# Performance work log

Measured on AMD Instinct MI355X. Metric: run time of the kernel, lower is better.

The kernel has to match this reference:

```python
import jax, jax.numpy as jnp
import numpy as np

DIM, D_INNER, D_STATE, DT_RANK, D_CONV = 1024, 2048, 16, 64, 4
BATCH, SEQ = 2, 1024

def setup_inputs() -> dict:
    key = jax.random.key(0)
    ks = jax.random.split(key, 9)
    s = 0.02
    A = jnp.tile(jnp.arange(1, D_STATE + 1, dtype=jnp.float32), (D_INNER, 1))
    return {
        "x": jax.random.normal(ks[0], (BATCH, SEQ, DIM), jnp.float32),
        "in_proj_w": jax.random.normal(ks[1], (DIM, 2 * D_INNER), jnp.float32) * s,
        "conv_w": jax.random.normal(ks[2], (D_INNER, 1, D_CONV), jnp.float32) * 0.2,
        "conv_b": jax.random.normal(ks[3], (D_INNER,), jnp.float32) * 0.1,
        "x_proj_w": jax.random.normal(ks[4], (D_INNER, DT_RANK + 2 * D_STATE), jnp.float32) * s,
        "dt_proj_w": jax.random.normal(ks[5], (DT_RANK, D_INNER), jnp.float32) * s,
        "dt_proj_b": jax.random.normal(ks[6], (D_INNER,), jnp.float32) * 0.1,
        "A_log": jnp.log(A),
        "D_param": jnp.ones((D_INNER,), jnp.float32),
        "out_proj_w": jax.random.normal(ks[7], (D_INNER, DIM), jnp.float32) * s,
    }

def _silu(v):
    return v * jax.nn.sigmoid(v)

def _ssm_forward(x, in_proj_w, conv_w, conv_b, x_proj_w, dt_proj_w, dt_proj_b, A_log, D_param, out_proj_w):
    b, l, _ = x.shape
    d_inner, d_conv = conv_w.shape[0], conv_w.shape[2]
    dt_rank, n = dt_proj_w.shape[0], A_log.shape[1]
    # input projection and split into conv branch / gate branch
    x_and_res = x @ in_proj_w                      # (b, l, 2*d_inner)
    xp, res = x_and_res[..., :d_inner], x_and_res[..., d_inner:]
    # causal depthwise conv (torch pads d_conv-1 both sides then slices [:l])
    h = jax.lax.conv_general_dilated(
        xp.transpose(0, 2, 1), conv_w,
        window_strides=(1,), padding=[(d_conv - 1, 0)],
        dimension_numbers=("NCH", "OIH", "NCH"),
        feature_group_count=d_inner,
    ) + conv_b[None, :, None]                      # (b, d_inner, l)
    h = _silu(h.transpose(0, 2, 1))                # (b, l, d_inner)
    # input-dependent SSM parameters
    A = -jnp.exp(A_log)                            # (d_inner, n)
    x_dbl = h @ x_proj_w                           # (b, l, dt_rank + 2n)
    dlt, Bm, Cm = (x_dbl[..., :dt_rank],
                   x_dbl[..., dt_rank:dt_rank + n],
                   x_dbl[..., dt_rank + n:])
    delta = jax.nn.softplus(dlt @ dt_proj_w + dt_proj_b)   # (b, l, d_inner)
    # discretization
    deltaA = jnp.exp(jnp.einsum("bld,dn->bldn", delta, A))             # (b,l,d,n)
    deltaB_u = (delta * h)[..., None] * Bm[:, :, None, :]              # (b,l,d,n)
    # sequential selective scan over time via lax.scan
    def step(state, t):
        dA_t, dBu_t, c_t = t
        state = dA_t * state + dBu_t               # (b, d, n)
        y_t = jnp.einsum("bdn,bn->bd", state, c_t)
        return state, y_t
    init = jnp.zeros((b, d_inner, n), h.dtype)
    _, ys = jax.lax.scan(step, init,
                         (deltaA.transpose(1, 0, 2, 3),
                          deltaB_u.transpose(1, 0, 2, 3),
                          Cm.transpose(1, 0, 2)))
    y = ys.transpose(1, 0, 2) + h * D_param        # (b, l, d_inner)
    y = y * _silu(res)
    return y @ out_proj_w                          # (b, l, dim)

def reference(x, in_proj_w, conv_w, conv_b, x_proj_w, dt_proj_w, dt_proj_b, A_log, D_param, out_proj_w):
    return _ssm_forward(x, in_proj_w, conv_w, conv_b, x_proj_w, dt_proj_w, dt_proj_b, A_log, D_param, out_proj_w)
```

## Files before the change

kernel.cpp:

```cpp
#include <hip/hip_runtime.h>
#include <hip/hip_bf16.h>

#define DIM     1024
#define DINNER  2048
#define NSTATE  16
#define DTRANK  64
#define DCONV   4
#define BATCH   2
#define SEQ     1024
#define BL      (BATCH*SEQ)
#define XDBLW   96
#define NCHUNK  32
#define TCHUNK  32
#define KSLICE  16
#define G4SK    4
#define LOG2E   1.44269504088896f
#define LN2     0.69314718055995f

typedef __attribute__((ext_vector_type(4))) float  f32x4;
typedef __attribute__((ext_vector_type(8))) short  bf16x8;
typedef unsigned short ushort_t;

__device__ __forceinline__ ushort_t f2bf(float f) {
    union { float f; unsigned int u; } v; v.f = f;
    unsigned int lsb = (v.u >> 16) & 1u;
    v.u += 0x7fffu + lsb;
    return (ushort_t)(v.u >> 16);
}
__device__ __forceinline__ float bf2f(ushort_t h) {
    union { unsigned u; float f; } v; v.u = ((unsigned)h) << 16; return v.f;
}
__device__ __forceinline__ float hexp2(float x) { return __builtin_amdgcn_exp2f(x); }
__device__ __forceinline__ float hlog2(float x) { return __builtin_amdgcn_logf(x); }
__device__ __forceinline__ float hrcp(float x)  { return __builtin_amdgcn_rcpf(x); }
__device__ __forceinline__ float softplus_fast(float x) {
    float e = hexp2(-fabsf(x) * LOG2E);
    return fmaxf(x, 0.f) + LN2 * hlog2(1.f + e);
}
__device__ __forceinline__ float sigmoid_fast(float x) {
    return hrcp(1.f + hexp2(-x * LOG2E));
}

typedef __attribute__((address_space(1))) unsigned int gu32_t;
typedef __attribute__((address_space(3))) unsigned int lu32_t;
__device__ __forceinline__ void gload_lds16(const ushort_t* g, ushort_t* l) {
    __builtin_amdgcn_global_load_lds((const gu32_t*)(const void*)g,
                                     (lu32_t*)(void*)l, 16, 0, 0);
}

__global__ __launch_bounds__(256) void prep_fused(
    const float* __restrict__ Win,  ushort_t* __restrict__ WtIn,
    const float* __restrict__ Wout, ushort_t* __restrict__ WtOut,
    const float* __restrict__ Wxp,  ushort_t* __restrict__ WtXp,
    const float* __restrict__ x,    ushort_t* __restrict__ xb)
{
    __shared__ float tile[32][33];
    const int tid = threadIdx.x;
    const int tx = tid & 31, ty = tid >> 5;
    const int bid = blockIdx.x;

    const float* src; ushort_t* dst; int R, C, bx, by;
    if (bid < 4096)      { src = Win;  dst = WtIn;  R = 1024; C = 4096; int j = bid;        bx = j % 128; by = j / 128; }
    else if (bid < 6144) { src = Wout; dst = WtOut; R = 2048; C = 1024; int j = bid - 4096; bx = j % 32;  by = j / 32; }
    else if (bid < 6336) { src = Wxp;  dst = WtXp;  R = 2048; C = 96;   int j = bid - 6144; bx = j % 3;   by = j / 3; }
    else {
        int i = ((bid - 6336) * 256 + tid) * 4;
        f32x4 v = *(const f32x4*)(x + i);
        ushort_t r0 = f2bf(v[0]), r1 = f2bf(v[1]), r2 = f2bf(v[2]), r3 = f2bf(v[3]);
        *(uint2*)(xb + i) = make_uint2((unsigned)r0 | ((unsigned)r1 << 16),
                                       (unsigned)r2 | ((unsigned)r3 << 16));
        return;
    }

    const int r0 = by * 32, c0 = bx * 32;
    #pragma unroll
    for (int i = 0; i < 4; ++i)
        tile[ty + i * 8][tx] = src[(size_t)(r0 + ty + i * 8) * C + c0 + tx];
    __syncthreads();
    #pragma unroll
    for (int i = 0; i < 4; ++i)
        dst[(size_t)(c0 + ty + i * 8) * R + r0 + tx] = f2bf(tile[tx][ty + i * 8]);
}

__global__ __launch_bounds__(256) void gemm_lds(
    const ushort_t* __restrict__ A,  int lda,
    const ushort_t* __restrict__ Bt, int ldb,
    int K,
    float* __restrict__ Cf, ushort_t* __restrict__ Cb, int ldc)
{
    __shared__ ushort_t As[2][128 * 32];
    __shared__ ushort_t Bs[2][128 * 32];

    const int tid  = threadIdx.x;
    const int m0   = blockIdx.y * 128;
    const int n0   = blockIdx.x * 128;
    const int wid  = tid >> 6;
    const int lane = tid & 63;
    const int wm   = (wid >> 1) * 64;
    const int wn   = (wid & 1) * 64;
    const int lr   = lane & 15;
    const int lk   = (lane >> 4) * 8;

    const int c0 = wid * 64 + lane;
    const int c1 = 256 + c0;
    const int r0 = c0 >> 2, f0 = (c0 & 3) * 8;
    const int r1 = c1 >> 2, f1 = (c1 & 3) * 8;
    const int lo0 = (wid * 64) * 8;
    const int lo1 = (256 + wid * 64) * 8;

    f32x4 acc[4][4];
    #pragma unroll
    for (int m = 0; m < 4; ++m)
        #pragma unroll
        for (int n = 0; n < 4; ++n)
            acc[m][n] = (f32x4){0.f, 0.f, 0.f, 0.f};

    const int nk = K >> 5;

    gload_lds16(A  + (size_t)(m0 + r0) * lda + f0, &As[0][lo0]);
    gload_lds16(A  + (size_t)(m0 + r1) * lda + f1, &As[0][lo1]);
    gload_lds16(Bt + (size_t)(n0 + r0) * ldb + f0, &Bs[0][lo0]);
    gload_lds16(Bt + (size_t)(n0 + r1) * ldb + f1, &Bs[0][lo1]);

    for (int k = 0; k < nk; ++k) {
        const int cur = k & 1;
        if (k + 1 < nk) {
            const int k0 = (k + 1) << 5;
            gload_lds16(A  + (size_t)(m0 + r0) * lda + k0 + f0, &As[cur ^ 1][lo0]);
            gload_lds16(A  + (size_t)(m0 + r1) * lda + k0 + f1, &As[cur ^ 1][lo1]);
            gload_lds16(Bt + (size_t)(n0 + r0) * ldb + k0 + f0, &Bs[cur ^ 1][lo0]);
            gload_lds16(Bt + (size_t)(n0 + r1) * ldb + k0 + f1, &Bs[cur ^ 1][lo1]);
            asm volatile("s_waitcnt vmcnt(4)" ::: "memory");
        } else {
            asm volatile("s_waitcnt vmcnt(0)" ::: "memory");
        }
        __builtin_amdgcn_sched_barrier(0);
        __builtin_amdgcn_s_barrier();

        bf16x8 af[4], bfr[4];
        #pragma unroll
        for (int m = 0; m < 4; ++m)
            af[m] = *(const bf16x8*)(&As[cur][(wm + m * 16 + lr) * 32 + lk]);
        #pragma unroll
        for (int n = 0; n < 4; ++n)
            bfr[n] = *(const bf16x8*)(&Bs[cur][(wn + n * 16 + lr) * 32 + lk]);

        #pragma unroll
        for (int m = 0; m < 4; ++m)
            #pragma unroll
            for (int n = 0; n < 4; ++n)
                acc[m][n] = __builtin_amdgcn_mfma_f32_16x16x32_bf16(af[m], bfr[n], acc[m][n], 0, 0, 0);
        __builtin_amdgcn_s_barrier();
    }

    const int rbase = (lane >> 4) * 4;
    #pragma unroll
    for (int m = 0; m < 4; ++m) {
        #pragma unroll
        for (int n = 0; n < 4; ++n) {
            int col = n0 + wn + n * 16 + lr;
            #pragma unroll
            for (int r = 0; r < 4; ++r) {
                int row = m0 + wm + m * 16 + rbase + r;
                float v = acc[m][n][r];
                if (Cf) Cf[(size_t)row * ldc + col] = v;
                if (Cb) Cb[(size_t)row * ldc + col] = f2bf(v);
            }
        }
    }
}

__global__ __launch_bounds__(256) void gemm_lds_sk(
    const ushort_t* __restrict__ A,  int lda,
    const ushort_t* __restrict__ Bt, int ldb,
    int klen,
    float* __restrict__ Part, int ldc, int mn)
{
    __shared__ ushort_t As[2][128 * 32];
    __shared__ ushort_t Bs[2][128 * 32];

    const int tid  = threadIdx.x;
    const int m0   = blockIdx.y * 128;
    const int n0   = blockIdx.x * 128;
    const int kb   = blockIdx.z * klen;
    float* Cf = Part + (size_t)blockIdx.z * mn;

    const int wid  = tid >> 6;
    const int lane = tid & 63;
    const int wm   = (wid >> 1) * 64;
    const int wn   = (wid & 1) * 64;
    const int lr   = lane & 15;
    const int lk   = (lane >> 4) * 8;

    const int c0 = wid * 64 + lane;
    const int c1 = 256 + c0;
    const int r0 = c0 >> 2, f0 = (c0 & 3) * 8;
    const int r1 = c1 >> 2, f1 = (c1 & 3) * 8;
    const int lo0 = (wid * 64) * 8;
    const int lo1 = (256 + wid * 64) * 8;

    f32x4 acc[4][4];
    #pragma unroll
    for (int m = 0; m < 4; ++m)
        #pragma unroll
        for (int n = 0; n < 4; ++n)
            acc[m][n] = (f32x4){0.f, 0.f, 0.f, 0.f};

    const int nk = klen >> 5;

    gload_lds16(A  + (size_t)(m0 + r0) * lda + kb + f0, &As[0][lo0]);
    gload_lds16(A  + (size_t)(m0 + r1) * lda + kb + f1, &As[0][lo1]);
    gload_lds16(Bt + (size_t)(n0 + r0) * ldb + kb + f0, &Bs[0][lo0]);
    gload_lds16(Bt + (size_t)(n0 + r1) * ldb + kb + f1, &Bs[0][lo1]);

    for (int k = 0; k < nk; ++k) {
        const int cur = k & 1;
        if (k + 1 < nk) {
            const int k0 = kb + ((k + 1) << 5);
            gload_lds16(A  + (size_t)(m0 + r0) * lda + k0 + f0, &As[cur ^ 1][lo0]);
            gload_lds16(A  + (size_t)(m0 + r1) * lda + k0 + f1, &As[cur ^ 1][lo1]);
            gload_lds16(Bt + (size_t)(n0 + r0) * ldb + k0 + f0, &Bs[cur ^ 1][lo0]);
            gload_lds16(Bt + (size_t)(n0 + r1) * ldb + k0 + f1, &Bs[cur ^ 1][lo1]);
            asm volatile("s_waitcnt vmcnt(4)" ::: "memory");
        } else {
            asm volatile("s_waitcnt vmcnt(0)" ::: "memory");
        }
        __builtin_amdgcn_sched_barrier(0);
        __builtin_amdgcn_s_barrier();

        bf16x8 af[4], bfr[4];
        #pragma unroll
        for (int m = 0; m < 4; ++m)
            af[m] = *(const bf16x8*)(&As[cur][(wm + m * 16 + lr) * 32 + lk]);
        #pragma unroll
        for (int n = 0; n < 4; ++n)
            bfr[n] = *(const bf16x8*)(&Bs[cur][(wn + n * 16 + lr) * 32 + lk]);

        #pragma unroll
        for (int m = 0; m < 4; ++m)
            #pragma unroll
            for (int n = 0; n < 4; ++n)
                acc[m][n] = __builtin_amdgcn_mfma_f32_16x16x32_bf16(af[m], bfr[n], acc[m][n], 0, 0, 0);
        __builtin_amdgcn_s_barrier();
    }

    const int rbase = (lane >> 4) * 4;
    #pragma unroll
    for (int m = 0; m < 4; ++m) {
        #pragma unroll
        for (int n = 0; n < 4; ++n) {
            int col = n0 + wn + n * 16 + lr;
            #pragma unroll
            for (int r = 0; r < 4; ++r) {
                int row = m0 + wm + m * 16 + rbase + r;
                Cf[(size_t)row * ldc + col] = acc[m][n][r];
            }
        }
    }
}

__global__ __launch_bounds__(256) void g4_reduce(
    const float* __restrict__ Part, float* __restrict__ out)
{
    int i = (blockIdx.x * 256 + threadIdx.x) * 4;
    const size_t mn = (size_t)BL * DIM;
    f32x4 s = *(const f32x4*)(Part + i);
    #pragma unroll
    for (int z = 1; z < G4SK; ++z)
        s += *(const f32x4*)(Part + z * mn + i);
    *(f32x4*)(out + i) = s;
}

__global__ __launch_bounds__(256) void gemm_n96_splitk(
    const ushort_t* __restrict__ A,
    const ushort_t* __restrict__ Bt,
    float* __restrict__ Ppart)
{
    __shared__ ushort_t As[128 * 40];
    __shared__ ushort_t Bs[96 * 40];

    const int tid   = threadIdx.x;
    const int ks    = blockIdx.x;
    const int m0    = blockIdx.y * 128;
    const int kbase = ks * (DINNER / KSLICE);
    const int wid   = tid >> 6;
    const int lane  = tid & 63;
    const int wm    = wid * 32;
    const int lr    = lane & 15;
    const int lk    = (lane >> 4) * 8;

    f32x4 acc[2][6];
    #pragma unroll
    for (int m = 0; m < 2; ++m)
        #pragma unroll
        for (int n = 0; n < 6; ++n)
            acc[m][n] = (f32x4){0.f, 0.f, 0.f, 0.f};

    for (int k0 = kbase; k0 < kbase + DINNER / KSLICE; k0 += 32) {
        #pragma unroll
        for (int c = 0; c < 2; ++c) {
            int cid = tid + c * 256;
            int row = cid >> 2, ck = (cid & 3) * 8;
            *(uint4*)(&As[row * 40 + ck]) =
                *(const uint4*)(A + (size_t)(m0 + row) * DINNER + k0 + ck);
        }
        {
            int row = tid >> 2, ck = (tid & 3) * 8;
            *(uint4*)(&Bs[row * 40 + ck]) =
                *(const uint4*)(Bt + (size_t)row * DINNER + k0 + ck);
            if (tid < 128) {
                int cid = 256 + tid;
                int row2 = cid >> 2, ck2 = (cid & 3) * 8;
                *(uint4*)(&Bs[row2 * 40 + ck2]) =
                    *(const uint4*)(Bt + (size_t)row2 * DINNER + k0 + ck2);
            }
        }
        __syncthreads();

        bf16x8 af[2], bfr[6];
        #pragma unroll
        for (int m = 0; m < 2; ++m)
            af[m] = *(const bf16x8*)(&As[(wm + m * 16 + lr) * 40 + lk]);
        #pragma unroll
        for (int n = 0; n < 6; ++n)
            bfr[n] = *(const bf16x8*)(&Bs[(n * 16 + lr) * 40 + lk]);

        #pragma unroll
        for (int m = 0; m < 2; ++m)
            #pragma unroll
            for (int n = 0; n < 6; ++n)
                acc[m][n] = __builtin_amdgcn_mfma_f32_16x16x32_bf16(af[m], bfr[n], acc[m][n], 0, 0, 0);
        __syncthreads();
    }

    const int rbase = (lane >> 4) * 4;
    #pragma unroll
    for (int m = 0; m < 2; ++m) {
        #pragma unroll
        for (int n = 0; n < 6; ++n) {
            int col = n * 16 + lr;
            #pragma unroll
            for (int r = 0; r < 4; ++r) {
                int row = m0 + wm + m * 16 + rbase + r;
                Ppart[((size_t)ks * BL + row) * XDBLW + col] = acc[m][n][r];
            }
        }
    }
}

__global__ __launch_bounds__(256) void g2_reduce(
    const float* __restrict__ Ppart, float* __restrict__ xdbl)
{
    int idx = blockIdx.x * 256 + threadIdx.x;
    int row = idx / 24, cg = (idx % 24) * 4;
    f32x4 s = (f32x4){0.f, 0.f, 0.f, 0.f};
    #pragma unroll
    for (int ks = 0; ks < KSLICE; ++ks)
        s += *(const f32x4*)(Ppart + ((size_t)ks * BL + row) * XDBLW + cg);
    *(f32x4*)(xdbl + (size_t)row * XDBLW + cg) = s;
}

__global__ __launch_bounds__(256, 4) void delta_v6(
    const float* __restrict__ xdbl,
    const float* __restrict__ Wdt,
    const float* __restrict__ dtb,
    ushort_t* __restrict__ delta_bf)
{
    __shared__ float WS[64][256];
    __shared__ float dS[32][64];
    const int tid  = threadIdx.x;
    const int d0   = (blockIdx.x & 7) * 256;
    const int row0 = (blockIdx.x >> 3) * 32;

    #pragma unroll
    for (int i = 0; i < 16; ++i) {
        int c = i * 256 + tid;
        int k = c >> 6, co = (c & 63) * 4;
        *(f32x4*)&WS[k][co] = *(const f32x4*)(Wdt + (size_t)k * DINNER + d0 + co);
    }
    #pragma unroll
    for (int i = 0; i < 2; ++i) {
        int c = i * 256 + tid;
        int r = c >> 4, co = (c & 15) * 4;
        *(f32x4*)&dS[r][co] = *(const f32x4*)(xdbl + (size_t)(row0 + r) * XDBLW + co);
    }
    __syncthreads();

    const int w    = tid >> 6;
    const int lane = tid & 63;
    const int dd   = lane * 4;

    f32x4 acc[8];
    {
        f32x4 bb = *(const f32x4*)(dtb + d0 + dd);
        #pragma unroll
        for (int r = 0; r < 8; ++r) acc[r] = bb;
    }

    for (int kq = 0; kq < 16; ++kq) {
        f32x4 dv[8];
        #pragma unroll
        for (int r = 0; r < 8; ++r)
            dv[r] = *(const f32x4*)&dS[w * 8 + r][kq * 4];
        #pragma unroll
        for (int kk = 0; kk < 4; ++kk) {
            f32x4 wv = *(const f32x4*)&WS[kq * 4 + kk][dd];
            #pragma unroll
            for (int r = 0; r < 8; ++r) {
                float dk = dv[r][kk];
                acc[r][0] = fmaf(dk, wv[0], acc[r][0]);
                acc[r][1] = fmaf(dk, wv[1], acc[r][1]);
                acc[r][2] = fmaf(dk, wv[2], acc[r][2]);
                acc[r][3] = fmaf(dk, wv[3], acc[r][3]);
            }
        }
    }

    #pragma unroll
    for (int r = 0; r < 8; ++r) {
        const size_t rowb = (size_t)(row0 + w * 8 + r) * DINNER + d0;
        f32x4 v = acc[r];
        ushort_t o[4];
        #pragma unroll
        for (int j = 0; j < 4; ++j)
            o[j] = f2bf(softplus_fast(v[j]));
        *(uint2*)(delta_bf + rowb + dd) = make_uint2(
            (unsigned)o[0] | ((unsigned)o[1] << 16), (unsigned)o[2] | ((unsigned)o[3] << 16));
    }
}

__global__ __launch_bounds__(256) void conv_silu(
    const ushort_t* __restrict__ xrb,
    const float* __restrict__ convw,
    const float* __restrict__ convb,
    ushort_t* __restrict__ hb)
{
    const int d  = blockIdx.x * 256 + threadIdx.x;
    const int bt = blockIdx.y;
    const int t  = bt & (SEQ - 1);

    float acc = convb[d];
    #pragma unroll
    for (int j = 0; j < DCONV; ++j) {
        int tt = t + j - (DCONV - 1);
        if (tt >= 0)
            acc += convw[d * DCONV + j] * bf2f(xrb[(size_t)(bt + j - (DCONV - 1)) * 4096 + d]);
    }
    float h = acc * sigmoid_fast(acc);
    hb[(size_t)bt * DINNER + d] = f2bf(h);
}

__global__ __launch_bounds__(256) void scan_p1(
    const ushort_t* __restrict__ delta_bf,
    const ushort_t* __restrict__ hb,
    const float* __restrict__ xdbl,
    const float* __restrict__ Alog,
    float* __restrict__ Pbuf,
    float* __restrict__ Sbuf)
{
    const int d  = (blockIdx.x & 7) * 256 + threadIdx.x;
    const int bc = blockIdx.x >> 3;
    const int b  = bc >> 5;
    const int c  = bc & (NCHUNK - 1);
    const int t0 = c * TCHUNK;

    float A[NSTATE];
    #pragma unroll
    for (int q = 0; q < 4; ++q) {
        f32x4 al = *(const f32x4*)(Alog + (size_t)d * NSTATE + q * 4);
        #pragma unroll
        for (int j = 0; j < 4; ++j)
            A[q * 4 + j] = -hexp2(al[j] * LOG2E) * LOG2E;
    }

    float s[NSTATE], pp[NSTATE];
    #pragma unroll
    for (int n = 0; n < NSTATE; ++n) { s[n] = 0.f; pp[n] = 1.f; }

    for (int tt = 0; tt < TCHUNK; ++tt) {
        const size_t row = (size_t)(b * SEQ + t0 + tt);
        float dl = bf2f(delta_bf[row * DINNER + d]);
        float hv = bf2f(hb[row * DINNER + d]);
        float dlh = dl * hv;
        float Bv[NSTATE];
        #pragma unroll
        for (int q = 0; q < 4; ++q) {
            f32x4 bv = *(const f32x4*)(xdbl + row * XDBLW + DTRANK + q * 4);
            #pragma unroll
            for (int j = 0; j < 4; ++j) Bv[q * 4 + j] = bv[j];
        }
        #pragma unroll
        for (int n = 0; n < NSTATE; ++n) {
            float a = hexp2(dl * A[n]);
            s[n]  = fmaf(a, s[n], dlh * Bv[n]);
            pp[n] *= a;
        }
    }

    const size_t o = (((size_t)b * NCHUNK + c) * DINNER + d) * NSTATE;
    #pragma unroll
    for (int q = 0; q < 4; ++q) {
        *(f32x4*)(Sbuf + o + q * 4) = (f32x4){s[q*4+0], s[q*4+1], s[q*4+2], s[q*4+3]};
        *(f32x4*)(Pbuf + o + q * 4) = (f32x4){pp[q*4+0], pp[q*4+1], pp[q*4+2], pp[q*4+3]};
    }
}

__global__ __launch_bounds__(256) void scan_p2(
    const float* __restrict__ Pbuf, float* __restrict__ Sbuf)
{
    const int tid = blockIdx.x * 256 + threadIdx.x;
    const int n = tid & 15;
    const int d = (tid >> 4) & (DINNER - 1);
    const int b = tid >> 15;
    const size_t stride = (size_t)DINNER * NSTATE;
    size_t idx = ((size_t)b * NCHUNK * DINNER + d) * NSTATE + n;
    float cin = 0.f;
    for (int c = 0; c < NCHUNK; ++c, idx += stride) {
        float S = Sbuf[idx];
        float P = Pbuf[idx];
        Sbuf[idx] = cin;
        cin = fmaf(P, cin, S);
    }
}

__global__ __launch_bounds__(256) void scan_p3(
    const ushort_t* __restrict__ delta_bf,
    const ushort_t* __restrict__ hb,
    const float* __restrict__ xdbl,
    const ushort_t* __restrict__ xrb,
    const float* __restrict__ Alog,
    const float* __restrict__ Dp,
    const float* __restrict__ Sbuf,
    ushort_t* __restrict__ yb)
{
    const int d  = (blockIdx.x & 7) * 256 + threadIdx.x;
    const int bc = blockIdx.x >> 3;
    const int b  = bc >> 5;
    const int c  = bc & (NCHUNK - 1);
    const int t0 = c * TCHUNK;

    float A[NSTATE];
    #pragma unroll
    for (int q = 0; q < 4; ++q) {
        f32x4 al = *(const f32x4*)(Alog + (size_t)d * NSTATE + q * 4);
        #pragma unroll
        for (int j = 0; j < 4; ++j)
            A[q * 4 + j] = -hexp2(al[j] * LOG2E) * LOG2E;
    }
    const float Dd = Dp[d];

    float s[NSTATE];
    const size_t o = (((size_t)b * NCHUNK + c) * DINNER + d) * NSTATE;
    #pragma unroll
    for (int q = 0; q < 4; ++q) {
        f32x4 sv = *(const f32x4*)(Sbuf + o + q * 4);
        #pragma unroll
        for (int j = 0; j < 4; ++j) s[q * 4 + j] = sv[j];
    }

    for (int tt = 0; tt < TCHUNK; ++tt) {
        const size_t row = (size_t)(b * SEQ + t0 + tt);
        float dl = bf2f(delta_bf[row * DINNER + d]);
        float hv = bf2f(hb[row * DINNER + d]);
        float rv = bf2f(xrb[row * 4096 + DINNER + d]);
        float dlh = dl * hv;
        float Bv[NSTATE], Cv[NSTATE];
        #pragma unroll
        for (int q = 0; q < 4; ++q) {
            f32x4 bv = *(const f32x4*)(xdbl + row * XDBLW + DTRANK + q * 4);
            f32x4 cv = *(const f32x4*)(xdbl + row * XDBLW + DTRANK + NSTATE + q * 4);
            #pragma unroll
            for (int j = 0; j < 4; ++j) { Bv[q*4+j] = bv[j]; Cv[q*4+j] = cv[j]; }
        }
        float y = 0.f;
        #pragma unroll
        for (int n = 0; n < NSTATE; ++n) {
            float a = hexp2(dl * A[n]);
            s[n] = fmaf(a, s[n], dlh * Bv[n]);
            y = fmaf(s[n], Cv[n], y);
        }
        y = fmaf(hv, Dd, y);
        y = y * rv * sigmoid_fast(rv);
        yb[row * DINNER + d] = f2bf(y);
    }
}

extern "C" void kernel_launch(void* const* d_in, const int* in_sizes, int n_in,
                              void* d_out, int out_size, void* d_ws, size_t ws_size,
                              hipStream_t stream)
{
    const float* x     = (const float*)d_in[0];
    const float* Win   = (const float*)d_in[1];
    const float* convw = (const float*)d_in[2];
    const float* convb = (const float*)d_in[3];
    const float* Wxp   = (const float*)d_in[4];
    const float* Wdt   = (const float*)d_in[5];
    const float* dtb   = (const float*)d_in[6];
    const float* Alog  = (const float*)d_in[7];
    const float* Dp    = (const float*)d_in[8];
    const float* Wout  = (const float*)d_in[9];
    float* out = (float*)d_out;

    char* base = (char*)d_ws; size_t off = 0;
    auto alloc = [&](size_t bytes) -> char* {
        char* q = base + off;
        off = (off + bytes + 255) & ~(size_t)255;
        return q;
    };
    ushort_t* WtIn   = (ushort_t*)alloc((size_t)4096 * 1024 * 2);
    ushort_t* WtOut  = (ushort_t*)alloc((size_t)1024 * 2048 * 2);
    ushort_t* WtXp   = (ushort_t*)alloc((size_t)96   * 2048 * 2);
    ushort_t* xb     = (ushort_t*)alloc((size_t)BL * DIM * 2);
    ushort_t* xrb    = (ushort_t*)alloc((size_t)BL * 4096 * 2);
    ushort_t* hb     = (ushort_t*)alloc((size_t)BL * DINNER * 2);
    float*    xdbl   = (float*)   alloc((size_t)BL * XDBLW * 4);
    ushort_t* dltbf  = (ushort_t*)alloc((size_t)BL * DINNER * 2);
    ushort_t* yb     = (ushort_t*)alloc((size_t)BL * DINNER * 2);
    float*    Pbuf   = (float*)   alloc((size_t)BATCH * NCHUNK * DINNER * NSTATE * 4);
    float*    Sbuf   = (float*)   alloc((size_t)BATCH * NCHUNK * DINNER * NSTATE * 4);
    float*    Ppart  = (float*)   alloc((size_t)KSLICE * BL * XDBLW * 4);
    float*    G4part = (float*)   alloc((size_t)G4SK * BL * DIM * 4);
    (void)ws_size;

    prep_fused<<<dim3(8384), 256, 0, stream>>>(Win, WtIn, Wout, WtOut, Wxp, WtXp, x, xb);

    gemm_lds<<<dim3(4096/128, BL/128), 256, 0, stream>>>(
        xb, DIM, WtIn, DIM, DIM, nullptr, xrb, 2*DINNER);

    conv_silu<<<dim3(DINNER/256, BL), 256, 0, stream>>>(xrb, convw, convb, hb);

    gemm_n96_splitk<<<dim3(KSLICE, BL/128), 256, 0, stream>>>(hb, WtXp, Ppart);
    g2_reduce<<<dim3(BL * 24 / 256), 256, 0, stream>>>(Ppart, xdbl);

    delta_v6<<<dim3(8 * (BL / 32)), 256, 0, stream>>>(xdbl, Wdt, dtb, dltbf);

    scan_p1<<<dim3(8 * BATCH * NCHUNK), 256, 0, stream>>>(dltbf, hb, xdbl, Alog, Pbuf, Sbuf);
    scan_p2<<<dim3(BATCH * DINNER * NSTATE / 256), 256, 0, stream>>>(Pbuf, Sbuf);
    scan_p3<<<dim3(8 * BATCH * NCHUNK), 256, 0, stream>>>(dltbf, hb, xdbl, xrb, Alog, Dp, Sbuf, yb);

    gemm_lds_sk<<<dim3(DIM/128, BL/128, G4SK), 256, 0, stream>>>(
        yb, DINNER, WtOut, DINNER, DINNER/G4SK, G4part, DIM, BL*DIM);
    g4_reduce<<<dim3(BL*DIM/4/256), 256, 0, stream>>>(G4part, out);
}
```

Before: 154.5 us.

## Double GEMM K-tile to 64 with XOR-swizzled LDS layout

Both bf16 MFMA GEMM kernels now stage 64-wide K slices per iteration instead of 32, halving the number of barrier/wait rounds per K sweep. The global-to-LDS copies use an XOR swizzle of the 16-byte column group by row, and fragment reads apply the matching swizzle to avoid LDS bank conflicts with the wider 128-byte rows. LDS use doubles to 64 KB per block, which may reduce occupancy. K lengths must now be multiples of 64, including split-K slice lengths.

```diff
diff --git a/kernel.cpp b/kernel.cpp
--- a/kernel.cpp
+++ b/kernel.cpp
@@ -88,8 +88,8 @@
     int K,
     float* __restrict__ Cf, ushort_t* __restrict__ Cb, int ldc)
 {
-    __shared__ ushort_t As[2][128 * 32];
-    __shared__ ushort_t Bs[2][128 * 32];
+    __shared__ ushort_t As[2][128 * 64];
+    __shared__ ushort_t Bs[2][128 * 64];
 
     const int tid  = threadIdx.x;
     const int m0   = blockIdx.y * 128;
@@ -99,14 +99,15 @@
     const int wm   = (wid >> 1) * 64;
     const int wn   = (wid & 1) * 64;
     const int lr   = lane & 15;
-    const int lk   = (lane >> 4) * 8;
-
-    const int c0 = wid * 64 + lane;
-    const int c1 = 256 + c0;
-    const int r0 = c0 >> 2, f0 = (c0 & 3) * 8;
-    const int r1 = c1 >> 2, f1 = (c1 & 3) * 8;
-    const int lo0 = (wid * 64) * 8;
-    const int lo1 = (256 + wid * 64) * 8;
+
+    int rq[4], gq[4], lo[4];
+    #pragma unroll
+    for (int q = 0; q < 4; ++q) {
+        int c = q * 256 + tid;
+        rq[q] = c >> 3;
+        gq[q] = ((c & 7) ^ (rq[q] & 7)) * 8;
+        lo[q] = (q * 256 + wid * 64) * 8;
+    }
 
     f32x4 acc[4][4];
     #pragma unroll
@@ -115,41 +116,47 @@
         for (int n = 0; n < 4; ++n)
             acc[m][n] = (f32x4){0.f, 0.f, 0.f, 0.f};
 
-    const int nk = K >> 5;
-
-    gload_lds16(A  + (size_t)(m0 + r0) * lda + f0, &As[0][lo0]);
-    gload_lds16(A  + (size_t)(m0 + r1) * lda + f1, &As[0][lo1]);
-    gload_lds16(Bt + (size_t)(n0 + r0) * ldb + f0, &Bs[0][lo0]);
-    gload_lds16(Bt + (size_t)(n0 + r1) * ldb + f1, &Bs[0][lo1]);
+    const int nk = K >> 6;
+
+    #pragma unroll
+    for (int q = 0; q < 4; ++q) {
+        gload_lds16(A  + (size_t)(m0 + rq[q]) * lda + gq[q], &As[0][lo[q]]);
+        gload_lds16(Bt + (size_t)(n0 + rq[q]) * ldb + gq[q], &Bs[0][lo[q]]);
+    }
 
     for (int k = 0; k < nk; ++k) {
         const int cur = k & 1;
         if (k + 1 < nk) {
-            const int k0 = (k + 1) << 5;
-            gload_lds16(A  + (size_t)(m0 + r0) * lda + k0 + f0, &As[cur ^ 1][lo0]);
-            gload_lds16(A  + (size_t)(m0 + r1) * lda + k0 + f1, &As[cur ^ 1][lo1]);
-            gload_lds16(Bt + (size_t)(n0 + r0) * ldb + k0 + f0, &Bs[cur ^ 1][lo0]);
-            gload_lds16(Bt + (size_t)(n0 + r1) * ldb + k0 + f1, &Bs[cur ^ 1][lo1]);
-            asm volatile("s_waitcnt vmcnt(4)" ::: "memory");
+            const int k0 = (k + 1) << 6;
+            #pragma unroll
+            for (int q = 0; q < 4; ++q) {
+                gload_lds16(A  + (size_t)(m0 + rq[q]) * lda + k0 + gq[q], &As[cur ^ 1][lo[q]]);
+                gload_lds16(Bt + (size_t)(n0 + rq[q]) * ldb + k0 + gq[q], &Bs[cur ^ 1][lo[q]]);
+            }
+            asm volatile("s_waitcnt vmcnt(8)" ::: "memory");
         } else {
             asm volatile("s_waitcnt vmcnt(0)" ::: "memory");
         }
         __builtin_amdgcn_sched_barrier(0);
         __builtin_amdgcn_s_barrier();
 
-        bf16x8 af[4], bfr[4];
-        #pragma unroll
-        for (int m = 0; m < 4; ++m)
-            af[m] = *(const bf16x8*)(&As[cur][(wm + m * 16 + lr) * 32 + lk]);
-        #pragma unroll
-        for (int n = 0; n < 4; ++n)
-            bfr[n] = *(const bf16x8*)(&Bs[cur][(wn + n * 16 + lr) * 32 + lk]);
-
-        #pragma unroll
-        for (int m = 0; m < 4; ++m)
+        #pragma unroll
+        for (int kk = 0; kk < 2; ++kk) {
+            const int lg = (lane >> 4) + kk * 4;
+            const int pc = (lg ^ (lr & 7)) * 8;
+            bf16x8 af[4], bfr[4];
+            #pragma unroll
+            for (int m = 0; m < 4; ++m)
+                af[m] = *(const bf16x8*)(&As[cur][(wm + m * 16 + lr) * 64 + pc]);
             #pragma unroll
             for (int n = 0; n < 4; ++n)
-                acc[m][n] = __builtin_amdgcn_mfma_f32_16x16x32_bf16(af[m], bfr[n], acc[m][n], 0, 0, 0);
+                bfr[n] = *(const bf16x8*)(&Bs[cur][(wn + n * 16 + lr) * 64 + pc]);
+            #pragma unroll
+            for (int m = 0; m < 4; ++m)
+                #pragma unroll
+                for (int n = 0; n < 4; ++n)
+                    acc[m][n] = __builtin_amdgcn_mfma_f32_16x16x32_bf16(af[m], bfr[n], acc[m][n], 0, 0, 0);
+        }
         __builtin_amdgcn_s_barrier();
     }
 
@@ -176,8 +183,8 @@
     int klen,
     float* __restrict__ Part, int ldc, int mn)
 {
-    __shared__ ushort_t As[2][128 * 32];
-    __shared__ ushort_t Bs[2][128 * 32];
+    __shared__ ushort_t As[2][128 * 64];
+    __shared__ ushort_t Bs[2][128 * 64];
 
     const int tid  = threadIdx.x;
     const int m0   = blockIdx.y * 128;
@@ -190,14 +197,15 @@
     const int wm   = (wid >> 1) * 64;
     const int wn   = (wid & 1) * 64;
     const int lr   = lane & 15;
-    const int lk   = (lane >> 4) * 8;
-
-    const int c0 = wid * 64 + lane;
-    const int c1 = 256 + c0;
-    const int r0 = c0 >> 2, f0 = (c0 & 3) * 8;
-    const int r1 = c1 >> 2, f1 = (c1 & 3) * 8;
-    const int lo0 = (wid * 64) * 8;
-    const int lo1 = (256 + wid * 64) * 8;
+
+    int rq[4], gq[4], lo[4];
+    #pragma unroll
+    for (int q = 0; q < 4; ++q) {
+        int c = q * 256 + tid;
+        rq[q] = c >> 3;
+        gq[q] = ((c & 7) ^ (rq[q] & 7)) * 8;
+        lo[q] = (q * 256 + wid * 64) * 8;
+    }
 
     f32x4 acc[4][4];
     #pragma unroll
@@ -206,41 +214,47 @@
         for (int n = 0; n < 4; ++n)
             acc[m][n] = (f32x4){0.f, 0.f, 0.f, 0.f};
 
-    const int nk = klen >> 5;
-
-    gload_lds16(A  + (size_t)(m0 + r0) * lda + kb + f0, &As[0][lo0]);
-    gload_lds16(A  + (size_t)(m0 + r1) * lda + kb + f1, &As[0][lo1]);
-    gload_lds16(Bt + (size_t)(n0 + r0) * ldb + kb + f0, &Bs[0][lo0]);
-    gload_lds16(Bt + (size_t)(n0 + r1) * ldb + kb + f1, &Bs[0][lo1]);
+    const int nk = klen >> 6;
+
+    #pragma unroll
+    for (int q = 0; q < 4; ++q) {
+        gload_lds16(A  + (size_t)(m0 + rq[q]) * lda + kb + gq[q], &As[0][lo[q]]);
+        gload_lds16(Bt + (size_t)(n0 + rq[q]) * ldb + kb + gq[q], &Bs[0][lo[q]]);
+    }
 
     for (int k = 0; k < nk; ++k) {
         const int cur = k & 1;
         if (k + 1 < nk) {
-            const int k0 = kb + ((k + 1) << 5);
-            gload_lds16(A  + (size_t)(m0 + r0) * lda + k0 + f0, &As[cur ^ 1][lo0]);
-            gload_lds16(A  + (size_t)(m0 + r1) * lda + k0 + f1, &As[cur ^ 1][lo1]);
-            gload_lds16(Bt + (size_t)(n0 + r0) * ldb + k0 + f0, &Bs[cur ^ 1][lo0]);
-            gload_lds16(Bt + (size_t)(n0 + r1) * ldb + k0 + f1, &Bs[cur ^ 1][lo1]);
-            asm volatile("s_waitcnt vmcnt(4)" ::: "memory");
+            const int k0 = kb + ((k + 1) << 6);
+            #pragma unroll
+            for (int q = 0; q < 4; ++q) {
+                gload_lds16(A  + (size_t)(m0 + rq[q]) * lda + k0 + gq[q], &As[cur ^ 1][lo[q]]);
+                gload_lds16(Bt + (size_t)(n0 + rq[q]) * ldb + k0 + gq[q], &Bs[cur ^ 1][lo[q]]);
+            }
+            asm volatile("s_waitcnt vmcnt(8)" ::: "memory");
         } else {
             asm volatile("s_waitcnt vmcnt(0)" ::: "memory");
         }
         __builtin_amdgcn_sched_barrier(0);
         __builtin_amdgcn_s_barrier();
 
-        bf16x8 af[4], bfr[4];
-        #pragma unroll
-        for (int m = 0; m < 4; ++m)
-            af[m] = *(const bf16x8*)(&As[cur][(wm + m * 16 + lr) * 32 + lk]);
-        #pragma unroll
-        for (int n = 0; n < 4; ++n)
-            bfr[n] = *(const bf16x8*)(&Bs[cur][(wn + n * 16 + lr) * 32 + lk]);
-
-        #pragma unroll
-        for (int m = 0; m < 4; ++m)
+        #pragma unroll
+        for (int kk = 0; kk < 2; ++kk) {
+            const int lg = (lane >> 4) + kk * 4;
+            const int pc = (lg ^ (lr & 7)) * 8;
+            bf16x8 af[4], bfr[4];
+            #pragma unroll
+            for (int m = 0; m < 4; ++m)
+                af[m] = *(const bf16x8*)(&As[cur][(wm + m * 16 + lr) * 64 + pc]);
             #pragma unroll
             for (int n = 0; n < 4; ++n)
-                acc[m][n] = __builtin_amdgcn_mfma_f32_16x16x32_bf16(af[m], bfr[n], acc[m][n], 0, 0, 0);
+                bfr[n] = *(const bf16x8*)(&Bs[cur][(wn + n * 16 + lr) * 64 + pc]);
+            #pragma unroll
+            for (int m = 0; m < 4; ++m)
+                #pragma unroll
+                for (int n = 0; n < 4; ++n)
+                    acc[m][n] = __builtin_amdgcn_mfma_f32_16x16x32_bf16(af[m], bfr[n], acc[m][n], 0, 0, 0);
+        }
         __builtin_amdgcn_s_barrier();
     }
 
```

After: 147.7 us. -4.4%, faster.
